# Optimization experiments

Hardware: AMD Instinct MI355X
Metric: run time of the kernel (lower is better)

## Reference

```python
import math
import jax, jax.numpy as jnp
import numpy as np

# ---- module hyperparameters (from init_kwargs) ----
BIG_K = 13
SMALL_K = 3
C_OUT = 128
GROUP_IN = 4
NK = math.ceil(BIG_K / SMALL_K)          # 5 small kernels cover the big one
C_IN = NK * C_OUT                        # 640
PADDING = SMALL_K - 1                    # shift() padding
EXTRA_PAD = PADDING - SMALL_K // 2       # 1
MID = BIG_K // 2
REAL_PAD = [MID - i * SMALL_K - PADDING for i in range(NK)]  # [4,1,-2,-5,-8]
MARGIN = BIG_K                           # zero-pad margin covering all shifts

B = 32
HOUT = 56
WOUT = 56
HIN = HOUT + 2 * EXTRA_PAD
WIN = WOUT + 2 * EXTRA_PAD


def _build_indices():
    # Faithful numpy replication of shuffle_idx_2_gen_pads (torch.manual_seed(123) analog).
    rng = np.random.RandomState(123)
    idx_offset = np.array(REAL_PAD * C_OUT, dtype=np.int32)  # (C_IN,)

    def group_pads():
        pads = []
        for _ in range(GROUP_IN):
            idx = np.concatenate([rng.permutation(NK) + i * NK for i in range(C_OUT)])
            pads.append(idx_offset[np.argsort(idx, kind='stable')])
        return np.stack(pads)  # (GROUP_IN, C_IN)

    pad_h = group_pads()
    pad_v = group_pads()
    pad_hv = np.concatenate([pad_h, pad_v], axis=0).T.astype(np.int32)  # (C_IN, 2*GROUP_IN)
    idx_identit = np.stack(
        [rng.randint(0, NK, C_OUT) + np.arange(C_OUT) * NK for _ in range(GROUP_IN)]
    ).T.astype(np.int32)  # (C_OUT, GROUP_IN)
    return pad_hv, idx_identit


def setup_inputs() -> dict:
    key = jax.random.key(0)
    pad_hv, idx_identit = _build_indices()
    x = jax.random.normal(key, (B, C_IN, HIN, WIN), dtype=jnp.float32)
    return {
        'x': x,
        'pad_hv': jnp.asarray(pad_hv),
        'idx_identit': jnp.asarray(idx_identit),
        'hout': HOUT,
        'wout': WOUT,
    }


def reference(x, pad_hv, idx_identit, hout, wout):
    # x: (B, C_IN, hout+2*EXTRA_PAD, wout+2*EXTRA_PAD)
    Bx = x.shape[0]
    M = MARGIN

    # ---- horizontal-shift branch: per-channel shift along W, accumulate over groups ----
    xp_w = jnp.pad(x, ((0, 0), (0, 0), (0, 0), (M, M)))          # zero pad width
    xh = xp_w[:, :, EXTRA_PAD:EXTRA_PAD + hout, :]
    w_base = jnp.arange(wout, dtype=jnp.int32) + EXTRA_PAD + M   # (wout,)
    out_h = jnp.zeros((Bx, C_IN, hout, wout), x.dtype)
    for g in range(GROUP_IN):
        idx = w_base[None, :] + pad_hv[:, g][:, None]            # (C_IN, wout)
        out_h = out_h + jnp.take_along_axis(xh, idx[None, :, None, :], axis=3)

    # ---- vertical-shift branch: per-channel shift along H ----
    xp_h = jnp.pad(x, ((0, 0), (0, 0), (M, M), (0, 0)))
    xv = xp_h[:, :, :, EXTRA_PAD:EXTRA_PAD + wout]               # (B,C_IN,HIN+2M,wout)
    h_base = jnp.arange(hout, dtype=jnp.int32) + EXTRA_PAD + M
    out_v = jnp.zeros((Bx, C_IN, hout, wout), x.dtype)
    for g in range(GROUP_IN):
        idx = h_base[None, :] + pad_hv[:, GROUP_IN + g][:, None]  # (C_IN, hout)
        out_v = out_v + jnp.take_along_axis(xv, idx[None, :, :, None], axis=2)

    # scatter-add input channels j into output channel idx_out[j] = j // NK
    out_h = out_h.reshape(Bx, C_OUT, NK, hout, wout).sum(axis=2)
    out_v = out_v.reshape(Bx, C_OUT, NK, hout, wout).sum(axis=2)

    # ---- identity branch: center crop + channel gather, summed over groups ----
    xc = x[:, :, EXTRA_PAD:EXTRA_PAD + hout, EXTRA_PAD:EXTRA_PAD + wout]
    out_id = xc[:, idx_identit, :, :].sum(axis=2)                # (B,C_OUT,hout,wout)

    return out_h, out_v, out_id
```

## Files before the change

### kernel.cpp

```cpp
#include <hip/hip_runtime.h>

#define BATCH   32
#define C_OUT_N 128
#define NK      5
#define C_IN_N  (NK * C_OUT_N)
#define HIN     58
#define WIN     58
#define HOUT    56
#define WOUT    56
#define NPIX    (HOUT * WOUT)
#define NTILE   (HOUT * (WOUT / 8))
#define OUT_PLANE ((size_t)BATCH * C_OUT_N * NPIX)

#define NTHREADS   512
#define LDS_STRIDE 70
#define LDS_ROWS   (NK * HIN)
#define LDS_HALVES (LDS_ROWS * LDS_STRIDE)
#define CH_STRIDE  (HIN * LDS_STRIDE)
#define NV4        (NK * HIN * WIN / 4)

typedef _Float16 h2 __attribute__((ext_vector_type(2)));

static __device__ __forceinline__ unsigned int h2u(h2 v) {
    unsigned int r; __builtin_memcpy(&r, &v, 4); return r;
}
static __device__ __forceinline__ h2 uh2(unsigned int u) {
    h2 r; __builtin_memcpy(&r, &u, 4); return r;
}
static __device__ __forceinline__ h2 algn(h2 lo, h2 hi) {
    return uh2(__builtin_amdgcn_alignbit(h2u(hi), h2u(lo), 16));
}
static __device__ __forceinline__ float uni(float v) {
    return __uint_as_float(__builtin_amdgcn_readfirstlane(__float_as_uint(v)));
}

__global__ __launch_bounds__(NTHREADS, 8) void addshift_pk_kernel(
    const float* __restrict__ x,
    const int*   __restrict__ pad_hv,
    const int*   __restrict__ idx_id,
    float*       __restrict__ out)
{
    extern __shared__ _Float16 lds[];

    const int bc  = blockIdx.x;
    const int b   = bc / C_OUT_N;
    const int co  = bc - b * C_OUT_N;
    const int tid = threadIdx.x;

    for (int i = tid; i < LDS_ROWS * 12; i += NTHREADS) {
        int j = i / 12;
        int m = i - j * 12;
        int c = (m < 7) ? m : (58 + m);
        lds[j * LDS_STRIDE + c] = (_Float16)0.f;
    }

    const float* xbase = x + (size_t)(b * C_IN_N + co * NK) * (HIN * WIN);
    for (int i = tid; i < NV4; i += NTHREADS) {
        int g = 4 * i;
        float4 v = *(const float4*)(xbase + g);
        int r = g / 58;
        int c = g - r * 58;
        _Float16* dst = &lds[r * LDS_STRIDE + 7 + c];
        if (c <= 54) {
            dst[0] = (_Float16)v.x;
            *(h2*)(dst + 1) = h2{(_Float16)v.y, (_Float16)v.z};
            dst[3] = (_Float16)v.w;
        } else {
            dst[0] = (_Float16)v.x;
            dst[1] = (_Float16)v.y;
            _Float16* d2 = &lds[(r + 1) * LDS_STRIDE + 7];
            d2[0] = (_Float16)v.z;
            d2[1] = (_Float16)v.w;
        }
    }

    float mhf[NK][5], mvf[NK][5], cntf[NK];
    #pragma unroll
    for (int k = 0; k < NK; ++k) {
        #pragma unroll
        for (int t = 0; t < 5; ++t) { mhf[k][t] = 0.f; mvf[k][t] = 0.f; }
        cntf[k] = 0.f;
        #pragma unroll
        for (int g = 0; g < 4; ++g) {
            int sh_v = pad_hv[(co * NK + k) * 8 + g];
            int th   = (4 - sh_v) / 3;
            int sv_v = pad_hv[(co * NK + k) * 8 + 4 + g];
            int tv   = (4 - sv_v) / 3;
            #pragma unroll
            for (int t = 0; t < 5; ++t) {
                mhf[k][t] += (th == t) ? 1.f : 0.f;
                mvf[k][t] += (tv == t) ? 1.f : 0.f;
            }
        }
    }
    #pragma unroll
    for (int g = 0; g < 4; ++g) {
        int c = idx_id[co * 4 + g] - co * NK;
        #pragma unroll
        for (int k = 0; k < NK; ++k) cntf[k] += (c == k) ? 1.f : 0.f;
    }
    #pragma unroll
    for (int k = 0; k < NK; ++k) {
        cntf[k] = uni(cntf[k]);
        #pragma unroll
        for (int t = 0; t < 5; ++t) { mhf[k][t] = uni(mhf[k][t]); mvf[k][t] = uni(mvf[k][t]); }
    }

    __syncthreads();

    const int q = tid;
    if (q < NTILE) {
        const int h  = q / 7;
        const int w0 = 8 * (q - h * 7);

        h2 sh[4], sv[4], si[4];
        #pragma unroll
        for (int m = 0; m < 4; ++m) {
            sh[m] = h2{(_Float16)0.f, (_Float16)0.f};
            sv[m] = sh[m]; si[m] = sh[m];
        }

        int  rcv[5];
        bool okv[5];
        #pragma unroll
        for (int t = 0; t < 5; ++t) {
            int rrow = h + 5 - 3 * t;
            rcv[t] = rrow < 0 ? 0 : (rrow > 57 ? 57 : rrow);
            okv[t] = (unsigned)rrow < 58u;
        }
        const int rowbase = (h + 1) * LDS_STRIDE + w0;

        #pragma unroll
        for (int k = 0; k < NK; ++k) {
            const _Float16* ch   = lds + k * CH_STRIDE;
            const _Float16* rowp = ch + rowbase;

            h2 H[10];
            #pragma unroll
            for (int m = 0; m < 10; ++m) H[m] = *(const h2*)(rowp + 2 * m);

            #pragma unroll
            for (int t = 0; t < 5; ++t) {
                float wg = mhf[k][t];
                if (wg != 0.f) {
                    _Float16 wh = (_Float16)wg;
                    h2 w2 = h2{wh, wh};
                    int j = 12 - 3 * t;
                    if ((j & 1) == 0) {
                        int m0 = j >> 1;
                        #pragma unroll
                        for (int m = 0; m < 4; ++m)
                            sh[m] += w2 * H[m0 + m];
                    } else {
                        int m0 = (j - 1) >> 1;
                        #pragma unroll
                        for (int m = 0; m < 4; ++m)
                            sh[m] += w2 * algn(H[m0 + m], H[m0 + m + 1]);
                    }
                }
            }

            float ck = cntf[k];
            if (ck != 0.f) {
                _Float16 ch16 = (_Float16)ck;
                h2 c2 = h2{ch16, ch16};
                #pragma unroll
                for (int m = 0; m < 4; ++m)
                    si[m] += c2 * H[4 + m];
            }

            #pragma unroll
            for (int t = 0; t < 5; ++t) {
                float wv = mvf[k][t];
                if (wv != 0.f) {
                    float wm = okv[t] ? wv : 0.f;
                    _Float16 wh = (_Float16)wm;
                    h2 w2 = h2{wh, wh};
                    const _Float16* vp = ch + rcv[t] * LDS_STRIDE + w0 + 8;
                    #pragma unroll
                    for (int m = 0; m < 4; ++m)
                        sv[m] += w2 * *(const h2*)(vp + 2 * m);
                }
            }
        }

        size_t o = (size_t)bc * NPIX + h * WOUT + w0;
        *(float4*)(out + o) =
            make_float4((float)sh[0].x, (float)sh[0].y, (float)sh[1].x, (float)sh[1].y);
        *(float4*)(out + o + 4) =
            make_float4((float)sh[2].x, (float)sh[2].y, (float)sh[3].x, (float)sh[3].y);
        *(float4*)(out + OUT_PLANE + o) =
            make_float4((float)sv[0].x, (float)sv[0].y, (float)sv[1].x, (float)sv[1].y);
        *(float4*)(out + OUT_PLANE + o + 4) =
            make_float4((float)sv[2].x, (float)sv[2].y, (float)sv[3].x, (float)sv[3].y);
        *(float4*)(out + 2 * OUT_PLANE + o) =
            make_float4((float)si[0].x, (float)si[0].y, (float)si[1].x, (float)si[1].y);
        *(float4*)(out + 2 * OUT_PLANE + o + 4) =
            make_float4((float)si[2].x, (float)si[2].y, (float)si[3].x, (float)si[3].y);
    }
}

extern "C" void kernel_launch(void* const* d_in, const int* in_sizes, int n_in,
                              void* d_out, int out_size, void* d_ws, size_t ws_size,
                              hipStream_t stream) {
    const float* x      = (const float*)d_in[0];
    const int*   pad_hv = (const int*)d_in[1];
    const int*   idx_id = (const int*)d_in[2];
    float*       out    = (float*)d_out;

    addshift_pk_kernel<<<dim3(BATCH * C_OUT_N), dim3(NTHREADS),
                         LDS_HALVES * 2, stream>>>(x, pad_hv, idx_id, out);
}
```

Before: 105.6 us.

## Make inner loop branchless with packed scalar weights and wider LDS reads

```diff
diff --git a/kernel.cpp b/kernel.cpp
--- a/kernel.cpp
+++ b/kernel.cpp
@@ -12,14 +12,16 @@
 #define NTILE   (HOUT * (WOUT / 8))
 #define OUT_PLANE ((size_t)BATCH * C_OUT_N * NPIX)
 
-#define NTHREADS   512
-#define LDS_STRIDE 70
-#define LDS_ROWS   (NK * HIN)
-#define LDS_HALVES (LDS_ROWS * LDS_STRIDE)
-#define CH_STRIDE  (HIN * LDS_STRIDE)
-#define NV4        (NK * HIN * WIN / 4)
+#define NTHREADS    512
+#define LDS_STRIDE  68
+#define ROWS_PER_CH 59
+#define CH_STRIDE   (ROWS_PER_CH * LDS_STRIDE)
+#define LDS_HALVES  (NK * CH_STRIDE)
+#define NV4         (NK * HIN * WIN / 4)
+#define ZMARG       (LDS_STRIDE + HIN * 10)
 
 typedef _Float16 h2 __attribute__((ext_vector_type(2)));
+typedef _Float16 h4 __attribute__((ext_vector_type(4)));
 
 static __device__ __forceinline__ unsigned int h2u(h2 v) {
     unsigned int r; __builtin_memcpy(&r, &v, 4); return r;
@@ -30,11 +32,12 @@
 static __device__ __forceinline__ h2 algn(h2 lo, h2 hi) {
     return uh2(__builtin_amdgcn_alignbit(h2u(hi), h2u(lo), 16));
 }
-static __device__ __forceinline__ float uni(float v) {
-    return __uint_as_float(__builtin_amdgcn_readfirstlane(__float_as_uint(v)));
-}
-
-__global__ __launch_bounds__(NTHREADS, 8) void addshift_pk_kernel(
+static __device__ __forceinline__ h2 pkrtz(float a, float b) {
+    auto t = __builtin_amdgcn_cvt_pkrtz(a, b);
+    h2 r; __builtin_memcpy(&r, &t, 4); return r;
+}
+
+__global__ __launch_bounds__(NTHREADS, 8) void addshift_bl_kernel(
     const float* __restrict__ x,
     const int*   __restrict__ pad_hv,
     const int*   __restrict__ idx_id,
@@ -47,28 +50,42 @@
     const int co  = bc - b * C_OUT_N;
     const int tid = threadIdx.x;
 
-    for (int i = tid; i < LDS_ROWS * 12; i += NTHREADS) {
-        int j = i / 12;
-        int m = i - j * 12;
-        int c = (m < 7) ? m : (58 + m);
-        lds[j * LDS_STRIDE + c] = (_Float16)0.f;
+    for (int i = tid; i < NK * ZMARG; i += NTHREADS) {
+        int k = i / ZMARG;
+        int m = i - k * ZMARG;
+        int idx;
+        if (m < LDS_STRIDE) {
+            idx = k * CH_STRIDE + 58 * LDS_STRIDE + m;
+        } else {
+            int mm  = m - LDS_STRIDE;
+            int row = mm / 10;
+            int c10 = mm - row * 10;
+            int c   = (c10 < 7) ? c10 : (58 + c10);
+            idx = k * CH_STRIDE + row * LDS_STRIDE + c;
+        }
+        lds[idx] = (_Float16)0.f;
     }
 
     const float* xbase = x + (size_t)(b * C_IN_N + co * NK) * (HIN * WIN);
     for (int i = tid; i < NV4; i += NTHREADS) {
         int g = 4 * i;
         float4 v = *(const float4*)(xbase + g);
-        int r = g / 58;
-        int c = g - r * 58;
-        _Float16* dst = &lds[r * LDS_STRIDE + 7 + c];
+        int r  = g / 58;
+        int c  = g - r * 58;
+        int k  = r / 58;
+        int lr = r - k * 58;
+        _Float16* dst = &lds[k * CH_STRIDE + lr * LDS_STRIDE + 7 + c];
         if (c <= 54) {
             dst[0] = (_Float16)v.x;
-            *(h2*)(dst + 1) = h2{(_Float16)v.y, (_Float16)v.z};
+            *(h2*)(dst + 1) = pkrtz(v.y, v.z);
             dst[3] = (_Float16)v.w;
         } else {
             dst[0] = (_Float16)v.x;
             dst[1] = (_Float16)v.y;
-            _Float16* d2 = &lds[(r + 1) * LDS_STRIDE + 7];
+            int r2 = r + 1;
+            int k2 = r2 / 58;
+            int l2 = r2 - k2 * 58;
+            _Float16* d2 = &lds[k2 * CH_STRIDE + l2 * LDS_STRIDE + 7];
             d2[0] = (_Float16)v.z;
             d2[1] = (_Float16)v.w;
         }
@@ -99,11 +116,20 @@
         #pragma unroll
         for (int k = 0; k < NK; ++k) cntf[k] += (c == k) ? 1.f : 0.f;
     }
+    unsigned int swh[NK][5], swv[NK][5], swc[NK];
     #pragma unroll
     for (int k = 0; k < NK; ++k) {
-        cntf[k] = uni(cntf[k]);
-        #pragma unroll
-        for (int t = 0; t < 5; ++t) { mhf[k][t] = uni(mhf[k][t]); mvf[k][t] = uni(mvf[k][t]); }
+        #pragma unroll
+        for (int t = 0; t < 5; ++t) {
+            _Float16 a  = (_Float16)mhf[k][t];
+            _Float16 b2 = (_Float16)mvf[k][t];
+            h2 pa = {a, a}, pb = {b2, b2};
+            swh[k][t] = __builtin_amdgcn_readfirstlane(h2u(pa));
+            swv[k][t] = __builtin_amdgcn_readfirstlane(h2u(pb));
+        }
+        _Float16 cc = (_Float16)cntf[k];
+        h2 pc = {cc, cc};
+        swc[k] = __builtin_amdgcn_readfirstlane(h2u(pc));
     }
 
     __syncthreads();
@@ -113,6 +139,15 @@
         const int h  = q / 7;
         const int w0 = 8 * (q - h * 7);
 
+        int voff[5];
+        #pragma unroll
+        for (int t = 0; t < 5; ++t) {
+            int rr = h + 5 - 3 * t;
+            int rv = ((unsigned)rr < 58u) ? rr : 58;
+            voff[t] = rv * LDS_STRIDE + w0 + 8;
+        }
+        const int rowbase = (h + 1) * LDS_STRIDE + w0;
+
         h2 sh[4], sv[4], si[4];
         #pragma unroll
         for (int m = 0; m < 4; ++m) {
@@ -120,67 +155,46 @@
             sv[m] = sh[m]; si[m] = sh[m];
         }
 
-        int  rcv[5];
-        bool okv[5];
-        #pragma unroll
-        for (int t = 0; t < 5; ++t) {
-            int rrow = h + 5 - 3 * t;
-            rcv[t] = rrow < 0 ? 0 : (rrow > 57 ? 57 : rrow);
-            okv[t] = (unsigned)rrow < 58u;
-        }
-        const int rowbase = (h + 1) * LDS_STRIDE + w0;
-
         #pragma unroll
         for (int k = 0; k < NK; ++k) {
-            const _Float16* ch   = lds + k * CH_STRIDE;
-            const _Float16* rowp = ch + rowbase;
+            const _Float16* chp  = lds + k * CH_STRIDE;
+            const _Float16* rowp = chp + rowbase;
 
             h2 H[10];
             #pragma unroll
-            for (int m = 0; m < 10; ++m) H[m] = *(const h2*)(rowp + 2 * m);
+            for (int m = 0; m < 5; ++m) {
+                h4 w = *(const h4*)(rowp + 4 * m);
+                __builtin_memcpy(&H[2 * m],     &w, 4);
+                __builtin_memcpy(&H[2 * m + 1], (const char*)&w + 4, 4);
+            }
+
+            #pragma unroll
+            for (int m = 0; m < 4; ++m) sh[m] += uh2(swh[k][4]) * H[m];
+            #pragma unroll
+            for (int m = 0; m < 4; ++m) sh[m] += uh2(swh[k][3]) * algn(H[1 + m], H[2 + m]);
+            #pragma unroll
+            for (int m = 0; m < 4; ++m) sh[m] += uh2(swh[k][2]) * H[3 + m];
+            #pragma unroll
+            for (int m = 0; m < 4; ++m) sh[m] += uh2(swh[k][1]) * algn(H[4 + m], H[5 + m]);
+            #pragma unroll
+            for (int m = 0; m < 4; ++m) sh[m] += uh2(swh[k][0]) * H[6 + m];
+
+            #pragma unroll
+            for (int m = 0; m < 4; ++m) si[m] += uh2(swc[k]) * H[4 + m];
 
             #pragma unroll
             for (int t = 0; t < 5; ++t) {
-                float wg = mhf[k][t];
-                if (wg != 0.f) {
-                    _Float16 wh = (_Float16)wg;
-                    h2 w2 = h2{wh, wh};
-                    int j = 12 - 3 * t;
-                    if ((j & 1) == 0) {
-                        int m0 = j >> 1;
-                        #pragma unroll
-                        for (int m = 0; m < 4; ++m)
-                            sh[m] += w2 * H[m0 + m];
-                    } else {
-                        int m0 = (j - 1) >> 1;
-                        #pragma unroll
-                        for (int m = 0; m < 4; ++m)
-                            sh[m] += w2 * algn(H[m0 + m], H[m0 + m + 1]);
-                    }
-                }
-            }
-
-            float ck = cntf[k];
-            if (ck != 0.f) {
-                _Float16 ch16 = (_Float16)ck;
-                h2 c2 = h2{ch16, ch16};
-                #pragma unroll
-                for (int m = 0; m < 4; ++m)
-                    si[m] += c2 * H[4 + m];
-            }
-
-            #pragma unroll
-            for (int t = 0; t < 5; ++t) {
-                float wv = mvf[k][t];
-                if (wv != 0.f) {
-                    float wm = okv[t] ? wv : 0.f;
-                    _Float16 wh = (_Float16)wm;
-                    h2 w2 = h2{wh, wh};
-                    const _Float16* vp = ch + rcv[t] * LDS_STRIDE + w0 + 8;
-                    #pragma unroll
-                    for (int m = 0; m < 4; ++m)
-                        sv[m] += w2 * *(const h2*)(vp + 2 * m);
-                }
+                const _Float16* vp = chp + voff[t];
+                h4 a  = *(const h4*)(vp);
+                h4 b4 = *(const h4*)(vp + 4);
+                h2 V0, V1, V2, V3;
+                __builtin_memcpy(&V0, &a, 4);
+                __builtin_memcpy(&V1, (const char*)&a + 4, 4);
+                __builtin_memcpy(&V2, &b4, 4);
+                __builtin_memcpy(&V3, (const char*)&b4 + 4, 4);
+                h2 wv = uh2(swv[k][t]);
+                sv[0] += wv * V0; sv[1] += wv * V1;
+                sv[2] += wv * V2; sv[3] += wv * V3;
             }
         }
 
@@ -208,6 +222,6 @@
     const int*   idx_id = (const int*)d_in[2];
     float*       out    = (float*)d_out;
 
-    addshift_pk_kernel<<<dim3(BATCH * C_OUT_N), dim3(NTHREADS),
+    addshift_bl_kernel<<<dim3(BATCH * C_OUT_N), dim3(NTHREADS),
                          LDS_HALVES * 2, stream>>>(x, pad_hv, idx_id, out);
 }
```

Result: slower. 110.6 us (+4.8%).
